# Kernel tuning notes

Hardware: AMD Instinct MI355X
Metric: run time of the kernel (lower is better)

## Reference

```python
import jax, jax.numpy as jnp
import numpy as np

OBS_LEN = 20
PRED_LEN = 30
H = 64          # h_dim
E = 16          # embedding_dim
B = 32768       # num_agents
IN_FEAT = OBS_LEN * 2  # 40
EPS = 1e-5


def layer_norm(x, g, b):
    m = jnp.mean(x, axis=-1, keepdims=True)
    v = jnp.mean((x - m) ** 2, axis=-1, keepdims=True)
    return (x - m) / jnp.sqrt(v + EPS) * g + b


def setup_inputs() -> dict:
    key = jax.random.key(0)
    ks = jax.random.split(key, 16)
    s = 0.1
    return {
        "traj_abs": jax.random.normal(ks[0], (OBS_LEN, B, 2), jnp.float32),
        "traj_rel": jax.random.normal(ks[1], (OBS_LEN, B, 2), jnp.float32),
        "decoder_h": jax.random.normal(ks[2], (1, B, H), jnp.float32),
        # LSTM params (PyTorch gate order: i, f, g, o)
        "W_ih": jax.random.normal(ks[3], (4 * H, E), jnp.float32) * s,
        "W_hh": jax.random.normal(ks[4], (4 * H, H), jnp.float32) * s,
        "b_ih": jax.random.normal(ks[5], (4 * H,), jnp.float32) * s,
        "b_hh": jax.random.normal(ks[6], (4 * H,), jnp.float32) * s,
        # spatial_embedding: Linear(40 -> 16)
        "emb_W": jax.random.normal(ks[7], (E, IN_FEAT), jnp.float32) * s,
        "emb_b": jax.random.normal(ks[8], (E,), jnp.float32) * s,
        # hidden2pos: Linear(64 -> 2)
        "h2p_W": jax.random.normal(ks[9], (2, H), jnp.float32) * s,
        "h2p_b": jax.random.normal(ks[10], (2,), jnp.float32) * s,
        # LayerNorms
        "ln1_g": jnp.ones((IN_FEAT,), jnp.float32),
        "ln1_b": jnp.zeros((IN_FEAT,), jnp.float32),
        "ln2_g": jnp.ones((H,), jnp.float32),
        "ln2_b": jnp.zeros((H,), jnp.float32),
    }


def reference(traj_abs, traj_rel, decoder_h, W_ih, W_hh, b_ih, b_hh,
              emb_W, emb_b, h2p_W, h2p_b, ln1_g, ln1_b, ln2_g, ln2_b):
    # use_rel_disp=False branch; D=1, num_layers=1 => LSTM is a single cell.
    h0 = decoder_h[0]                      # (B, H)
    c0 = jnp.zeros_like(h0)

    def step(carry, _):
        traj, h, c = carry
        # faithful to torch .view(num_agents, -1): raw row-major reshape (20,B,2)->(B,40)
        x = jax.nn.leaky_relu(
            layer_norm(traj.reshape(B, IN_FEAT), ln1_g, ln1_b) @ emb_W.T + emb_b
        )  # (B, E)
        gates = x @ W_ih.T + b_ih + h @ W_hh.T + b_hh   # (B, 4H)
        i, f, g, o = jnp.split(gates, 4, axis=-1)
        c = jax.nn.sigmoid(f) * c + jax.nn.sigmoid(i) * jnp.tanh(g)
        h = jax.nn.sigmoid(o) * jnp.tanh(c)
        pos = layer_norm(h, ln2_g, ln2_b) @ h2p_W.T + h2p_b  # (B, 2)
        traj = jnp.concatenate([traj[1:], pos[None]], axis=0)  # roll -1 on dim 0, set last
        return (traj, h, c), pos

    _, pred = jax.lax.scan(step, (traj_abs, h0, c0), None, length=PRED_LEN)
    return pred  # (PRED_LEN, B, 2)
```

## Files before the change

kernel.cpp:

```cpp
#include <hip/hip_runtime.h>
#include <hip/hip_bf16.h>

#define NAGENTS 32768
#define SLAB    65536
#define SPLIT   1310720
#define SPLIT4  327680
#define PRED    30
#define IN_F    40
#define LN_EPS  1e-5f
#define APB     64
#define NBLK    (NAGENTS/APB)
#define BTH     512
#define XSTRIDE 104
#define RSTR    72


typedef short bf16x8 __attribute__((ext_vector_type(8)));
typedef short bf16x4 __attribute__((ext_vector_type(4)));
typedef float f32x4  __attribute__((ext_vector_type(4)));

#define C_SGW  0
#define C_BW   16
#define C_G2   32
#define C_SG2  160
#define C_B2   162
#define C_BIAS 164
#define C_TOT  420

__device__ __forceinline__ float frcp(float x){ return __builtin_amdgcn_rcpf(x); }
__device__ __forceinline__ float fsigmoid(float x){ return frcp(1.f + __expf(-x)); }
__device__ __forceinline__ float ftanh(float x){
    float t = __expf(-2.f*fabsf(x));
    float r = (1.f - t) * frcp(1.f + t);
    return copysignf(r, x);
}
__device__ __forceinline__ float lrelu(float x){ return x > 0.f ? x : 0.01f*x; }
__device__ __forceinline__ short f2bf(float x){
    unsigned u = __float_as_uint(x);
    return (short)((u + 0x7FFFu + ((u>>16)&1u)) >> 16);
}
__device__ __forceinline__ float bf2f(short s){
    return __uint_as_float(((unsigned)(unsigned short)s) << 16);
}
__device__ __forceinline__ unsigned pk_bf16(float a, float b){
    __hip_bfloat162 h = __float22bfloat162_rn(float2{a, b});
    return *reinterpret_cast<unsigned*>(&h);
}

__global__ __launch_bounds__(BTH, 4)
void persist_kernel(const float* __restrict__ traj,
                    float* __restrict__ out,
                    const float* __restrict__ dec_h,
                    const float* __restrict__ W_ih, const float* __restrict__ W_hh,
                    const float* __restrict__ b_ih, const float* __restrict__ b_hh,
                    const float* __restrict__ emb_W, const float* __restrict__ emb_b,
                    const float* __restrict__ h2p_W, const float* __restrict__ h2p_b,
                    const float* __restrict__ ln1_g, const float* __restrict__ ln1_b,
                    const float* __restrict__ ln2_g, const float* __restrict__ ln2_b,
                    int* __restrict__ flags)
{
    __shared__ short Rs[APB*RSTR];
    __shared__ short Xs[APB*XSTRIDE];
    __shared__ float Ds[APB*16];
    __shared__ float St[APB*2];
    __shared__ float cst[C_TOT];

    const int tid  = threadIdx.x;
    const int bid  = blockIdx.x;
    const int a0   = bid * APB;
    const int l    = tid & 63;
    const int wv   = tid >> 6;
    const int gang = wv >> 2;
    const int wvin = wv & 3;
    const int cl   = l & 15;
    const int kb   = l >> 4;
    const int nh   = wvin*16 + cl;

    if (tid < 16) {
        int e = tid;
        float s = 0.f, b = 0.f;
        for (int f = 0; f < IN_F; ++f) {
            float wf = emb_W[e*40 + f];
            s += ln1_g[f] * wf;
            b += ln1_b[f] * wf;
        }
        cst[C_SGW + e] = s;
        cst[C_BW + e]  = b + emb_b[e];
    }
    if (tid < 128) {
        int k = tid >> 1, d = tid & 1;
        cst[C_G2 + tid] = ln2_g[k] * h2p_W[d*64 + k];
    }
    if (tid < 2) {
        int d = tid;
        float s = 0.f, b = 0.f;
        for (int k = 0; k < 64; ++k) {
            float wf = h2p_W[d*64 + k];
            s += ln2_g[k] * wf;
            b += ln2_b[k] * wf;
        }
        cst[C_SG2 + d] = s;
        cst[C_B2 + d]  = b + h2p_b[d];
    }
    if (tid >= 256) cst[C_BIAS + tid - 256] = b_ih[tid-256] + b_hh[tid-256];

    bf16x8 bw[4][3];
#pragma unroll
    for (int g = 0; g < 4; ++g)
#pragma unroll
        for (int ks = 0; ks < 3; ++ks) {
            int n = g*64 + nh;
            bf16x8 v;
#pragma unroll
            for (int j = 0; j < 8; ++j) {
                int k = ks*32 + kb*8 + j;
                float f = 0.f;
                if (k < 16)      f = W_ih[n*16 + k];
                else if (k < 80) f = W_hh[n*64 + (k-16)];
                v[j] = f2bf(f);
            }
            bw[g][ks] = v;
        }

    bf16x8 ew[2];
#pragma unroll
    for (int ks = 0; ks < 2; ++ks) {
        bf16x8 v;
#pragma unroll
        for (int j = 0; j < 8; ++j) {
            int k = ks*32 + kb*8 + j;
            float f = (k < IN_F) ? ln1_g[k] * emb_W[cl*40 + k] : 0.f;
            v[j] = f2bf(f);
        }
        ew[ks] = v;
    }

    for (int i = tid; i < APB*16; i += BTH) {
        int a = i >> 4, q = i & 15;
        float4 hv = ((const float4*)dec_h)[(a0 + a)*16 + q];
        uint2 pv{ pk_bf16(hv.x, hv.y), pk_bf16(hv.z, hv.w) };
        *(uint2*)&Xs[a*XSTRIDE + 16 + q*4] = pv;
    }
    if (tid < APB*2) {
        int a = tid >> 1, hf = tid & 1;
        *(bf16x8*)&Xs[a*XSTRIDE + 80 + hf*8] = bf16x8{0,0,0,0,0,0,0,0};
    }
    if (tid < APB*3) {
        int a = tid / 3, seg = tid - a*3;
        *(bf16x8*)&Rs[a*RSTR + 40 + seg*8] = bf16x8{0,0,0,0,0,0,0,0};
    }

    float cs[2][4];
#pragma unroll
    for (int mt = 0; mt < 2; ++mt)
#pragma unroll
        for (int r = 0; r < 4; ++r) cs[mt][r] = 0.f;

    __syncthreads();

    for (int s = 0; s < PRED; ++s) {
        {
            const long Ob = (long)s*SLAB + (long)a0*IN_F - SPLIT;
            const long Oe = Ob + APB*IN_F;
            if (Oe > 0) {
                long o0 = Ob < 0 ? 0 : Ob;
                int i0 = (int)(o0 >> 7);
                int i1 = (int)((Oe - 1) >> 7);
                for (int i = i0 + tid; i <= i1; i += BTH) {
                    int t = i >> 9, p = i & 511;
                    while (__hip_atomic_load(&flags[p], __ATOMIC_ACQUIRE,
                                             __HIP_MEMORY_SCOPE_AGENT) < t + 1)
                        __builtin_amdgcn_s_sleep(1);
                }
            }
        }
        __syncthreads();

        {
            const int Gb4 = s*(SLAB/4) + bid*(APB*IN_F/4);
            for (int i = tid; i < APB*IN_F/4; i += BTH) {
                int a = i / 10, f4 = i - a*10;
                int G4 = Gb4 + i;
                float4 v = (G4 < SPLIT4) ? ((const float4*)traj)[G4]
                                         : ((const float4*)out)[G4 - SPLIT4];
                uint2 pv{ pk_bf16(v.x, v.y), pk_bf16(v.z, v.w) };
                *(uint2*)&Rs[a*RSTR + f4*4] = pv;
            }
        }
        __syncthreads();

        if (wv < 4) {
            f32x4 dacc = f32x4{0.f, 0.f, 0.f, 0.f};
            const short* base = &Rs[(wv*16 + cl)*RSTR + kb*8];
            bf16x8 a0f = *(const bf16x8*)(base);
            bf16x8 a1f = *(const bf16x8*)(base + 32);
            dacc = __builtin_amdgcn_mfma_f32_16x16x32_bf16(a0f, ew[0], dacc, 0, 0, 0);
            dacc = __builtin_amdgcn_mfma_f32_16x16x32_bf16(a1f, ew[1], dacc, 0, 0, 0);
#pragma unroll
            for (int r = 0; r < 4; ++r)
                Ds[(wv*16 + kb*4 + r)*16 + cl] = dacc[r];
        } else {
            int t2 = tid - 256;
            int a = t2 >> 2, p = t2 & 3;
            const bf16x8* rp = (const bf16x8*)&Rs[a*RSTR + p*16];
            bf16x8 v0 = rp[0], v1 = rp[1];
            float s1 = 0.f, s2 = 0.f;
#pragma unroll
            for (int j = 0; j < 8; ++j) {
                float f0 = bf2f(v0[j]), f1 = bf2f(v1[j]);
                s1 += f0 + f1; s2 += f0*f0 + f1*f1;
            }
            s1 += __shfl_xor(s1, 1, 64); s2 += __shfl_xor(s2, 1, 64);
            s1 += __shfl_xor(s1, 2, 64); s2 += __shfl_xor(s2, 2, 64);
            if (p == 0) {
                float m = s1 * (1.f/IN_F);
                St[a*2]   = m;
                St[a*2+1] = rsqrtf(s2*(1.f/IN_F) - m*m + LN_EPS);
            }
        }
        __syncthreads();

        {
            int a = tid >> 3, p = tid & 7, e0 = p*2;
            float m = St[a*2], inv = St[a*2+1];
            float D0 = Ds[a*16 + e0], D1 = Ds[a*16 + e0 + 1];
            float x0 = inv*(D0 - m*cst[C_SGW+e0  ]) + cst[C_BW+e0  ];
            float x1 = inv*(D1 - m*cst[C_SGW+e0+1]) + cst[C_BW+e0+1];
            unsigned pv = pk_bf16(lrelu(x0), lrelu(x1));
            *(unsigned*)&Xs[a*XSTRIDE + e0] = pv;
        }
        __syncthreads();

        f32x4 acc[2][4];
#pragma unroll
        for (int g = 0; g < 4; ++g) {
            float bb = cst[C_BIAS + g*64 + nh];
            acc[0][g] = f32x4{bb, bb, bb, bb};
            acc[1][g] = f32x4{bb, bb, bb, bb};
        }
#pragma unroll
        for (int mt = 0; mt < 2; ++mt) {
            const short* base = &Xs[(gang*32 + mt*16 + cl)*XSTRIDE + kb*8];
            bf16x8 af0 = *(const bf16x8*)(base);
            bf16x8 af1 = *(const bf16x8*)(base + 32);
            bf16x8 af2 = *(const bf16x8*)(base + 64);
#pragma unroll
            for (int g = 0; g < 4; ++g) {
                acc[mt][g] = __builtin_amdgcn_mfma_f32_16x16x32_bf16(af0, bw[g][0], acc[mt][g], 0, 0, 0);
                acc[mt][g] = __builtin_amdgcn_mfma_f32_16x16x32_bf16(af1, bw[g][1], acc[mt][g], 0, 0, 0);
                acc[mt][g] = __builtin_amdgcn_mfma_f32_16x16x32_bf16(af2, bw[g][2], acc[mt][g], 0, 0, 0);
            }
        }
        __syncthreads();

#pragma unroll
        for (int mt = 0; mt < 2; ++mt) {
            int abase = gang*32 + mt*16 + kb*4;
#pragma unroll
            for (int r = 0; r < 4; ++r) {
                float cn = fsigmoid(acc[mt][1][r]) * cs[mt][r]
                         + fsigmoid(acc[mt][0][r]) * ftanh(acc[mt][2][r]);
                float hn = fsigmoid(acc[mt][3][r]) * ftanh(cn);
                cs[mt][r] = cn;
                Xs[(abase + r)*XSTRIDE + 16 + nh] = f2bf(hn);
            }
        }
        __syncthreads();

        {
            int a = tid >> 3, p = tid & 7;
            bf16x8 hv = *(const bf16x8*)&Xs[a*XSTRIDE + 16 + p*8];
            float s1 = 0.f, s2 = 0.f, d0 = 0.f, d1 = 0.f;
#pragma unroll
            for (int j = 0; j < 8; ++j) {
                float f = bf2f(hv[j]);
                float2 gw = *(const float2*)&cst[C_G2 + (p*8 + j)*2];
                s1 += f; s2 += f*f;
                d0 += f*gw.x; d1 += f*gw.y;
            }
#pragma unroll
            for (int mk = 1; mk < 8; mk <<= 1) {
                s1 += __shfl_xor(s1, mk, 64);
                s2 += __shfl_xor(s2, mk, 64);
                d0 += __shfl_xor(d0, mk, 64);
                d1 += __shfl_xor(d1, mk, 64);
            }
            if (p < 2) {
                float m   = s1 * (1.f/64);
                float inv = rsqrtf(s2*(1.f/64) - m*m + LN_EPS);
                float dd  = (p == 0) ? d0 : d1;
                float val = inv*(dd - m*cst[C_SG2+p]) + cst[C_B2+p];
                __hip_atomic_store(&out[s*SLAB + (a0 + a)*2 + p], val,
                                   __ATOMIC_RELAXED, __HIP_MEMORY_SCOPE_AGENT);
            }
        }

        if (s != PRED-1) {
            __syncthreads();
            if (tid == 0)
                __hip_atomic_store(&flags[bid], s+1, __ATOMIC_RELAXED,
                                   __HIP_MEMORY_SCOPE_AGENT);
        }
    }
}

extern "C" void kernel_launch(void* const* d_in, const int* in_sizes, int n_in,
                              void* d_out, int out_size, void* d_ws, size_t ws_size,
                              hipStream_t stream) {
    const float* traj  = (const float*)d_in[0];
    const float* dec_h = (const float*)d_in[2];
    const float* W_ih  = (const float*)d_in[3];
    const float* W_hh  = (const float*)d_in[4];
    const float* b_ih  = (const float*)d_in[5];
    const float* b_hh  = (const float*)d_in[6];
    const float* emb_W = (const float*)d_in[7];
    const float* emb_b = (const float*)d_in[8];
    const float* h2p_W = (const float*)d_in[9];
    const float* h2p_b = (const float*)d_in[10];
    const float* ln1_g = (const float*)d_in[11];
    const float* ln1_b = (const float*)d_in[12];
    const float* ln2_g = (const float*)d_in[13];
    const float* ln2_b = (const float*)d_in[14];
    float* out = (float*)d_out;
    int*   flg = (int*)d_ws;

    persist_kernel<<<NBLK, BTH, 0, stream>>>(
        traj, out, dec_h, W_ih, W_hh, b_ih, b_hh, emb_W, emb_b,
        h2p_W, h2p_b, ln1_g, ln1_b, ln2_g, ln2_b, flg);
}
```

Measured before the change: 311.8 us.

## Overlap recurrent h-GEMM with trajectory load and embedding in fused stage

```diff
diff --git a/kernel.cpp b/kernel.cpp
--- a/kernel.cpp
+++ b/kernel.cpp
@@ -12,11 +12,10 @@
 #define NBLK    (NAGENTS/APB)
 #define BTH     512
 #define XSTRIDE 104
-#define RSTR    72
+
 
 
 typedef short bf16x8 __attribute__((ext_vector_type(8)));
-typedef short bf16x4 __attribute__((ext_vector_type(4)));
 typedef float f32x4  __attribute__((ext_vector_type(4)));
 
 #define C_SGW  0
@@ -41,10 +40,6 @@
 }
 __device__ __forceinline__ float bf2f(short s){
     return __uint_as_float(((unsigned)(unsigned short)s) << 16);
-}
-__device__ __forceinline__ unsigned pk_bf16(float a, float b){
-    __hip_bfloat162 h = __float22bfloat162_rn(float2{a, b});
-    return *reinterpret_cast<unsigned*>(&h);
 }
 
 __global__ __launch_bounds__(BTH, 4)
@@ -59,9 +54,7 @@
                     const float* __restrict__ ln2_g, const float* __restrict__ ln2_b,
                     int* __restrict__ flags)
 {
-    __shared__ short Rs[APB*RSTR];
     __shared__ short Xs[APB*XSTRIDE];
-    __shared__ float Ds[APB*16];
     __shared__ float St[APB*2];
     __shared__ float cst[C_TOT];
 
@@ -115,8 +108,8 @@
             for (int j = 0; j < 8; ++j) {
                 int k = ks*32 + kb*8 + j;
                 float f = 0.f;
-                if (k < 16)      f = W_ih[n*16 + k];
-                else if (k < 80) f = W_hh[n*64 + (k-16)];
+                if (k < 64)      f = W_hh[n*64 + k];
+                else if (k < 80) f = W_ih[n*16 + (k-64)];
                 v[j] = f2bf(f);
             }
             bw[g][ks] = v;
@@ -138,17 +131,15 @@
     for (int i = tid; i < APB*16; i += BTH) {
         int a = i >> 4, q = i & 15;
         float4 hv = ((const float4*)dec_h)[(a0 + a)*16 + q];
-        uint2 pv{ pk_bf16(hv.x, hv.y), pk_bf16(hv.z, hv.w) };
-        *(uint2*)&Xs[a*XSTRIDE + 16 + q*4] = pv;
+        __hip_bfloat162 p0 = __float22bfloat162_rn(float2{hv.x, hv.y});
+        __hip_bfloat162 p1 = __float22bfloat162_rn(float2{hv.z, hv.w});
+        uint2 pv{ *reinterpret_cast<unsigned*>(&p0), *reinterpret_cast<unsigned*>(&p1) };
+        *(uint2*)&Xs[a*XSTRIDE + q*4] = pv;
     }
     if (tid < APB*2) {
         int a = tid >> 1, hf = tid & 1;
         *(bf16x8*)&Xs[a*XSTRIDE + 80 + hf*8] = bf16x8{0,0,0,0,0,0,0,0};
     }
-    if (tid < APB*3) {
-        int a = tid / 3, seg = tid - a*3;
-        *(bf16x8*)&Rs[a*RSTR + 40 + seg*8] = bf16x8{0,0,0,0,0,0,0,0};
-    }
 
     float cs[2][4];
 #pragma unroll
@@ -159,78 +150,6 @@
     __syncthreads();
 
     for (int s = 0; s < PRED; ++s) {
-        {
-            const long Ob = (long)s*SLAB + (long)a0*IN_F - SPLIT;
-            const long Oe = Ob + APB*IN_F;
-            if (Oe > 0) {
-                long o0 = Ob < 0 ? 0 : Ob;
-                int i0 = (int)(o0 >> 7);
-                int i1 = (int)((Oe - 1) >> 7);
-                for (int i = i0 + tid; i <= i1; i += BTH) {
-                    int t = i >> 9, p = i & 511;
-                    while (__hip_atomic_load(&flags[p], __ATOMIC_ACQUIRE,
-                                             __HIP_MEMORY_SCOPE_AGENT) < t + 1)
-                        __builtin_amdgcn_s_sleep(1);
-                }
-            }
-        }
-        __syncthreads();
-
-        {
-            const int Gb4 = s*(SLAB/4) + bid*(APB*IN_F/4);
-            for (int i = tid; i < APB*IN_F/4; i += BTH) {
-                int a = i / 10, f4 = i - a*10;
-                int G4 = Gb4 + i;
-                float4 v = (G4 < SPLIT4) ? ((const float4*)traj)[G4]
-                                         : ((const float4*)out)[G4 - SPLIT4];
-                uint2 pv{ pk_bf16(v.x, v.y), pk_bf16(v.z, v.w) };
-                *(uint2*)&Rs[a*RSTR + f4*4] = pv;
-            }
-        }
-        __syncthreads();
-
-        if (wv < 4) {
-            f32x4 dacc = f32x4{0.f, 0.f, 0.f, 0.f};
-            const short* base = &Rs[(wv*16 + cl)*RSTR + kb*8];
-            bf16x8 a0f = *(const bf16x8*)(base);
-            bf16x8 a1f = *(const bf16x8*)(base + 32);
-            dacc = __builtin_amdgcn_mfma_f32_16x16x32_bf16(a0f, ew[0], dacc, 0, 0, 0);
-            dacc = __builtin_amdgcn_mfma_f32_16x16x32_bf16(a1f, ew[1], dacc, 0, 0, 0);
-#pragma unroll
-            for (int r = 0; r < 4; ++r)
-                Ds[(wv*16 + kb*4 + r)*16 + cl] = dacc[r];
-        } else {
-            int t2 = tid - 256;
-            int a = t2 >> 2, p = t2 & 3;
-            const bf16x8* rp = (const bf16x8*)&Rs[a*RSTR + p*16];
-            bf16x8 v0 = rp[0], v1 = rp[1];
-            float s1 = 0.f, s2 = 0.f;
-#pragma unroll
-            for (int j = 0; j < 8; ++j) {
-                float f0 = bf2f(v0[j]), f1 = bf2f(v1[j]);
-                s1 += f0 + f1; s2 += f0*f0 + f1*f1;
-            }
-            s1 += __shfl_xor(s1, 1, 64); s2 += __shfl_xor(s2, 1, 64);
-            s1 += __shfl_xor(s1, 2, 64); s2 += __shfl_xor(s2, 2, 64);
-            if (p == 0) {
-                float m = s1 * (1.f/IN_F);
-                St[a*2]   = m;
-                St[a*2+1] = rsqrtf(s2*(1.f/IN_F) - m*m + LN_EPS);
-            }
-        }
-        __syncthreads();
-
-        {
-            int a = tid >> 3, p = tid & 7, e0 = p*2;
-            float m = St[a*2], inv = St[a*2+1];
-            float D0 = Ds[a*16 + e0], D1 = Ds[a*16 + e0 + 1];
-            float x0 = inv*(D0 - m*cst[C_SGW+e0  ]) + cst[C_BW+e0  ];
-            float x1 = inv*(D1 - m*cst[C_SGW+e0+1]) + cst[C_BW+e0+1];
-            unsigned pv = pk_bf16(lrelu(x0), lrelu(x1));
-            *(unsigned*)&Xs[a*XSTRIDE + e0] = pv;
-        }
-        __syncthreads();
-
         f32x4 acc[2][4];
 #pragma unroll
         for (int g = 0; g < 4; ++g) {
@@ -238,21 +157,96 @@
             acc[0][g] = f32x4{bb, bb, bb, bb};
             acc[1][g] = f32x4{bb, bb, bb, bb};
         }
+
+        if (wv < 4) {
+            const long Ob = (long)s*SLAB + (long)(a0 + wv*16)*40 - SPLIT;
+            if (Ob + 640 > 0) {
+                long o0 = Ob < 0 ? 0 : Ob;
+                int i0 = (int)(o0 >> 7);
+                int i1 = (int)((Ob + 639) >> 7);
+                if (l <= i1 - i0) {
+                    int i = i0 + l;
+                    int t = i >> 9, p = i & 511;
+                    while (__hip_atomic_load(&flags[p], __ATOMIC_RELAXED,
+                                             __HIP_MEMORY_SCOPE_AGENT) < t + 1)
+                        __builtin_amdgcn_s_sleep(1);
+                }
+                __builtin_amdgcn_fence(__ATOMIC_ACQUIRE, "agent");
+            }
+            int row = wv*16 + cl;
+            long V4 = (long)s*(SLAB/4) + (long)(a0 + row)*10 + kb*2;
+            float4 v0 = (V4 < SPLIT4) ? ((const float4*)traj)[V4]
+                                      : ((const float4*)out)[V4 - SPLIT4];
+            float4 v1 = (V4+1 < SPLIT4) ? ((const float4*)traj)[V4+1]
+                                        : ((const float4*)out)[V4+1 - SPLIT4];
+            float4 v2{0.f,0.f,0.f,0.f}, v3{0.f,0.f,0.f,0.f};
+            if (kb == 0) {
+                long V8 = V4 + 8;
+                v2 = (V8 < SPLIT4) ? ((const float4*)traj)[V8]
+                                   : ((const float4*)out)[V8 - SPLIT4];
+                v3 = (V8+1 < SPLIT4) ? ((const float4*)traj)[V8+1]
+                                     : ((const float4*)out)[V8+1 - SPLIT4];
+            }
+#pragma unroll
+            for (int mt = 0; mt < 2; ++mt) {
+                const short* hb = &Xs[(gang*32 + mt*16 + cl)*XSTRIDE + kb*8];
+                bf16x8 hf0 = *(const bf16x8*)(hb);
+                bf16x8 hf1 = *(const bf16x8*)(hb + 32);
+#pragma unroll
+                for (int g = 0; g < 4; ++g) {
+                    acc[mt][g] = __builtin_amdgcn_mfma_f32_16x16x32_bf16(hf0, bw[g][0], acc[mt][g], 0, 0, 0);
+                    acc[mt][g] = __builtin_amdgcn_mfma_f32_16x16x32_bf16(hf1, bw[g][1], acc[mt][g], 0, 0, 0);
+                }
+            }
+            float s1 = v0.x+v0.y+v0.z+v0.w + v1.x+v1.y+v1.z+v1.w
+                     + v2.x+v2.y+v2.z+v2.w + v3.x+v3.y+v3.z+v3.w;
+            float s2 = v0.x*v0.x+v0.y*v0.y+v0.z*v0.z+v0.w*v0.w
+                     + v1.x*v1.x+v1.y*v1.y+v1.z*v1.z+v1.w*v1.w
+                     + v2.x*v2.x+v2.y*v2.y+v2.z*v2.z+v2.w*v2.w
+                     + v3.x*v3.x+v3.y*v3.y+v3.z*v3.z+v3.w*v3.w;
+            s1 += __shfl_xor(s1, 16, 64); s2 += __shfl_xor(s2, 16, 64);
+            s1 += __shfl_xor(s1, 32, 64); s2 += __shfl_xor(s2, 32, 64);
+            if (kb == 0) {
+                float m = s1 * (1.f/IN_F);
+                St[(wv*16 + cl)*2]     = m;
+                St[(wv*16 + cl)*2 + 1] = rsqrtf(s2*(1.f/IN_F) - m*m + LN_EPS);
+            }
+            bf16x8 a0f{f2bf(v0.x),f2bf(v0.y),f2bf(v0.z),f2bf(v0.w),
+                       f2bf(v1.x),f2bf(v1.y),f2bf(v1.z),f2bf(v1.w)};
+            bf16x8 a1f{f2bf(v2.x),f2bf(v2.y),f2bf(v2.z),f2bf(v2.w),
+                       f2bf(v3.x),f2bf(v3.y),f2bf(v3.z),f2bf(v3.w)};
+            f32x4 dacc = f32x4{0.f, 0.f, 0.f, 0.f};
+            dacc = __builtin_amdgcn_mfma_f32_16x16x32_bf16(a0f, ew[0], dacc, 0, 0, 0);
+            dacc = __builtin_amdgcn_mfma_f32_16x16x32_bf16(a1f, ew[1], dacc, 0, 0, 0);
+#pragma unroll
+            for (int r = 0; r < 4; ++r) {
+                int rw = wv*16 + kb*4 + r;
+                float2 st = *(const float2*)&St[rw*2];
+                float xv = st.y*(dacc[r] - st.x*cst[C_SGW+cl]) + cst[C_BW+cl];
+                Xs[rw*XSTRIDE + 64 + cl] = f2bf(lrelu(xv));
+            }
+        } else {
+#pragma unroll
+            for (int mt = 0; mt < 2; ++mt) {
+                const short* hb = &Xs[(gang*32 + mt*16 + cl)*XSTRIDE + kb*8];
+                bf16x8 hf0 = *(const bf16x8*)(hb);
+                bf16x8 hf1 = *(const bf16x8*)(hb + 32);
+#pragma unroll
+                for (int g = 0; g < 4; ++g) {
+                    acc[mt][g] = __builtin_amdgcn_mfma_f32_16x16x32_bf16(hf0, bw[g][0], acc[mt][g], 0, 0, 0);
+                    acc[mt][g] = __builtin_amdgcn_mfma_f32_16x16x32_bf16(hf1, bw[g][1], acc[mt][g], 0, 0, 0);
+                }
+            }
+        }
+        __syncthreads();
+
 #pragma unroll
         for (int mt = 0; mt < 2; ++mt) {
-            const short* base = &Xs[(gang*32 + mt*16 + cl)*XSTRIDE + kb*8];
-            bf16x8 af0 = *(const bf16x8*)(base);
-            bf16x8 af1 = *(const bf16x8*)(base + 32);
-            bf16x8 af2 = *(const bf16x8*)(base + 64);
-#pragma unroll
-            for (int g = 0; g < 4; ++g) {
-                acc[mt][g] = __builtin_amdgcn_mfma_f32_16x16x32_bf16(af0, bw[g][0], acc[mt][g], 0, 0, 0);
-                acc[mt][g] = __builtin_amdgcn_mfma_f32_16x16x32_bf16(af1, bw[g][1], acc[mt][g], 0, 0, 0);
-                acc[mt][g] = __builtin_amdgcn_mfma_f32_16x16x32_bf16(af2, bw[g][2], acc[mt][g], 0, 0, 0);
-            }
-        }
-        __syncthreads();
-
+            bf16x8 xf = *(const bf16x8*)&Xs[(gang*32 + mt*16 + cl)*XSTRIDE + 64 + kb*8];
+#pragma unroll
+            for (int g = 0; g < 4; ++g)
+                acc[mt][g] = __builtin_amdgcn_mfma_f32_16x16x32_bf16(xf, bw[g][2], acc[mt][g], 0, 0, 0);
+        }
 #pragma unroll
         for (int mt = 0; mt < 2; ++mt) {
             int abase = gang*32 + mt*16 + kb*4;
@@ -262,14 +256,14 @@
                          + fsigmoid(acc[mt][0][r]) * ftanh(acc[mt][2][r]);
                 float hn = fsigmoid(acc[mt][3][r]) * ftanh(cn);
                 cs[mt][r] = cn;
-                Xs[(abase + r)*XSTRIDE + 16 + nh] = f2bf(hn);
+                Xs[(abase + r)*XSTRIDE + nh] = f2bf(hn);
             }
         }
         __syncthreads();
 
         {
             int a = tid >> 3, p = tid & 7;
-            bf16x8 hv = *(const bf16x8*)&Xs[a*XSTRIDE + 16 + p*8];
+            bf16x8 hv = *(const bf16x8*)&Xs[a*XSTRIDE + p*8];
             float s1 = 0.f, s2 = 0.f, d0 = 0.f, d1 = 0.f;
 #pragma unroll
             for (int j = 0; j < 8; ++j) {
```

After: 483.3 us. 55.0% more time.
